# Kernel optimization log

Hardware: AMD Instinct MI355X
Metric: run time of the kernel (lower is better)

The kernel has to match this reference:

```python
import jax, jax.numpy as jnp
import numpy as np

N_NODES = 50000
N_EDGES = 640000
D = 128
L = 3


def setup_inputs() -> dict:
    key = jax.random.key(0)
    k1, k2, k3, k4 = jax.random.split(key, 4)
    x = jax.random.normal(k1, (N_NODES, D), dtype=jnp.float32)
    # Glorot-ish scale so activations stay O(1) across 3 layers
    Ws = jax.random.normal(k2, (L, D, D), dtype=jnp.float32) * (1.0 / np.sqrt(D))
    bs = jnp.zeros((L, D), dtype=jnp.float32)
    edge_src = jax.random.randint(k3, (N_EDGES,), 0, N_NODES, dtype=jnp.int32)
    edge_dst = jax.random.randint(k4, (N_EDGES,), 0, N_NODES, dtype=jnp.int32)
    return {"x": x, "Ws": Ws, "bs": bs, "edge_src": edge_src, "edge_dst": edge_dst}


def reference(x, Ws, bs, edge_src, edge_dst):
    n = x.shape[0]
    ones = jnp.ones(edge_src.shape[0], dtype=x.dtype)
    # degrees, clamped to 1 as in dgl GraphConv(norm='both')
    deg_out = jnp.maximum(jax.ops.segment_sum(ones, edge_src, num_segments=n), 1.0)
    deg_in = jnp.maximum(jax.ops.segment_sum(ones, edge_dst, num_segments=n), 1.0)
    inv_sqrt_out = jax.lax.rsqrt(deg_out)[:, None]  # [N,1]
    inv_sqrt_in = jax.lax.rsqrt(deg_in)[:, None]    # [N,1]
    for l in range(Ws.shape[0]):
        h = x * inv_sqrt_out                         # src normalization
        msg = h[edge_src]                            # [E,D] gather
        agg = jax.ops.segment_sum(msg, edge_dst, num_segments=n)  # [N,D] scatter-add
        h = agg * inv_sqrt_in                        # dst normalization
        x = jax.nn.relu(h @ Ws[l] + bs[l])           # linear + ReLU
    return x
```

## Files before the change

### kernel.cpp

```cpp
#include <hip/hip_runtime.h>
#include <hip/hip_fp16.h>

typedef __attribute__((ext_vector_type(8))) _Float16 half8;
typedef __attribute__((ext_vector_type(4))) float f32x4;
typedef unsigned int u32;
typedef unsigned short u16;
typedef unsigned long long u64;

#define ELL_PAD 64
#define BKT 128
#define BKT_SH 7
#define EPB 2048
#define NAMAX 512
#define RUNCAP 3072


__global__ __launch_bounds__(256) void initpack(int* __restrict__ deg_out,
                                                u32* __restrict__ xz0,
                                                u32* __restrict__ xz1,
                                                const float* __restrict__ Ws,
                                                _Float16* __restrict__ Whi,
                                                _Float16* __restrict__ Wlo,
                                                int N, int padU32, int zb, int packTotal) {
  int b = blockIdx.x;
  if (b < zb) {
    int i = b * 256 + threadIdx.x;
    if (i < N) deg_out[i] = 0;
    if (b == 0) {
      for (int j = threadIdx.x; j < padU32; j += 256) { xz0[j] = 0; xz1[j] = 0; }
    }
    return;
  }
  int i = (b - zb) * 256 + threadIdx.x;
  if (i < packTotal) {
    int lane  = i & 63;
    int kstep = (i >> 6) & 3;
    int ntile = (i >> 8) & 7;
    int layer = i >> 11;
    int nn = ntile * 16 + (lane & 15);
    int k0 = kstep * 32 + (lane >> 4) * 8;
    const float* W = Ws + (size_t)layer * 128 * 128;
    size_t base = (size_t)i * 8;
    for (int j = 0; j < 8; j++) {
      float v = W[(k0 + j) * 128 + nn];
      _Float16 hi = (_Float16)v;
      Whi[base + j] = hi;
      Wlo[base + j] = (_Float16)(v - (float)hi);
    }
  }
}


__global__ __launch_bounds__(512) void parta(const int* __restrict__ esrc,
                                             const int* __restrict__ edst,
                                             int* __restrict__ deg_out,
                                             u32* __restrict__ part,
                                             u32* __restrict__ runTab,
                                             int E, int NB) {
  __shared__ u32 hist[512];
  __shared__ u32 stage[EPB];
  __shared__ u32 scanA[512];
  int a = blockIdx.x;
  int e0 = a * EPB;
  int e1 = min(E, e0 + EPB);
  int len = e1 - e0;
  int tid = threadIdx.x;
  if (tid <= NB) hist[tid] = 0;
  __syncthreads();
  for (int i = e0 + tid; i < e1; i += 512) {
    int s = esrc[i];
    int d = edst[i];
    atomicAdd(&deg_out[s], 1);
    atomicAdd(&hist[d >> BKT_SH], 1u);
  }
  __syncthreads();
  u32 myc = (tid < NB) ? hist[tid] : 0;
  scanA[tid] = myc;
  __syncthreads();
  for (int off = 1; off < NB; off <<= 1) {
    u32 t = scanA[tid] + ((tid >= off) ? scanA[tid - off] : 0);
    __syncthreads();
    scanA[tid] = t;
    __syncthreads();
  }
  u32 excl = scanA[tid] - myc;
  u32* rt = runTab + (size_t)a * (NB + 1);
  if (tid < NB) { rt[tid] = excl; hist[tid] = excl; }
  if (tid == 0) rt[NB] = (u32)len;
  __syncthreads();
  for (int i = e0 + tid; i < e1; i += 512) {
    int s = esrc[i];
    int d = edst[i];
    u32 p = atomicAdd(&hist[d >> BKT_SH], 1u);
    stage[p] = (u32)s | ((u32)(d & (BKT - 1)) << 16);
  }
  __syncthreads();
  u32* op = part + (size_t)a * EPB;
  for (int j = tid; j < len; j += 512) op[j] = stage[j];
}


__global__ __launch_bounds__(512) void partb(const u32* __restrict__ part,
                                             const u32* __restrict__ runTab,
                                             int* __restrict__ deg_in,
                                             u16* __restrict__ ell,
                                             int N, int NA, int NB) {
  __shared__ u16 slice[BKT * ELL_PAD];
  __shared__ u32 cnt2[BKT * 17];
  __shared__ u32 roff[NAMAX + 1];
  __shared__ u32 rbase[NAMAX];
  __shared__ u16 runid[RUNCAP];
  __shared__ u32 pstage[RUNCAP];
  __shared__ u32 scanA[512];
  int b = blockIdx.x;
  int base = b * BKT;
  int hi = min(BKT, N - base);
  if (hi <= 0) return;
  int tid = threadIdx.x;

  u32 nv = ((u32)N << 16) | (u32)N;
  u32* s32 = (u32*)slice;
  for (int j = tid; j < BKT * (ELL_PAD / 2); j += 512) s32[j] = nv;
  for (int j = tid; j < BKT * 17; j += 512) cnt2[j] = 0;
  u32 mylen = 0;
  if (tid < NA) {
    u32 s = runTab[(size_t)tid * (NB + 1) + b];
    u32 e = runTab[(size_t)tid * (NB + 1) + b + 1];
    mylen = e - s;
    rbase[tid] = (u32)tid * EPB + s;
  }
  scanA[tid] = mylen;
  __syncthreads();
  for (int off = 1; off < NA + 1; off <<= 1) {
    u32 t = scanA[tid] + ((tid >= off) ? scanA[tid - off] : 0);
    __syncthreads();
    scanA[tid] = t;
    __syncthreads();
  }
  if (tid <= NA) roff[tid] = scanA[tid] - mylen;
  __syncthreads();
  int T = (int)roff[NA];
  for (int a = tid; a < NA; a += 512) {
    u32 s0 = roff[a];
    u32 l  = roff[a + 1] - s0;
    for (u32 k = 0; k < l; k++)
      if (s0 + k < RUNCAP) runid[s0 + k] = (u16)a;
  }
  __syncthreads();
  for (int i = tid; i < T; i += 512) {
    int a;
    if (i < RUNCAP) a = runid[i];
    else {
      int lo = 0, hh = NA;
      while (hh - lo > 1) { int mid = (lo + hh) >> 1; if (roff[mid] <= (u32)i) lo = mid; else hh = mid; }
      a = lo;
    }
    u32 pair = part[(size_t)rbase[a] + ((u32)i - roff[a])];
    if (i < RUNCAP) pstage[i] = pair;
    u32 dl  = pair >> 16;
    u32 src = pair & 0xFFFFu;
    atomicAdd(&cnt2[dl * 17 + (src >> 12)], 1u);
  }
  __syncthreads();
  if (tid < BKT) {
    u32 run = 0;
    for (int bk = 0; bk < 16; bk++) {
      u32 t = cnt2[tid * 17 + bk];
      cnt2[tid * 17 + bk] = run;
      run += t;
    }
    if (tid < hi) deg_in[base + tid] = (int)run;
  }
  __syncthreads();
  for (int i = tid; i < T; i += 512) {
    u32 pair;
    if (i < RUNCAP) pair = pstage[i];
    else {
      int lo = 0, hh = NA;
      while (hh - lo > 1) { int mid = (lo + hh) >> 1; if (roff[mid] <= (u32)i) lo = mid; else hh = mid; }
      pair = part[(size_t)rbase[lo] + ((u32)i - roff[lo])];
    }
    u32 dl  = pair >> 16;
    u32 src = pair & 0xFFFFu;
    u32 p = atomicAdd(&cnt2[dl * 17 + (src >> 12)], 1u);
    if (p < ELL_PAD) slice[dl * ELL_PAD + p] = (u16)src;
  }
  __syncthreads();
  u32* eg = (u32*)(ell + (size_t)base * ELL_PAD);
  for (int j = tid; j < hi * (ELL_PAD / 2); j += 512) eg[j] = s32[j];
}


__global__ __launch_bounds__(256) void xscale(const float* __restrict__ x,
                                              const int* __restrict__ deg_out,
                                              __half2* __restrict__ xh, int n64) {
  int gid = blockIdx.x * 256 + threadIdx.x;
  if (gid >= n64) return;
  int row = gid >> 6;
  int d = deg_out[row]; if (d < 1) d = 1;
  float s = rsqrtf((float)d);
  float2 v = ((const float2*)x)[gid];
  xh[gid] = __floats2half2_rn(v.x * s, v.y * s);
}


__global__ __launch_bounds__(512) void layer16(const _Float16* __restrict__ xh,
                                               const int* __restrict__ deg_in,
                                               const u16* __restrict__ ell,
                                               const _Float16* __restrict__ Whi,
                                               const _Float16* __restrict__ Wlo,
                                               const float* __restrict__ bias,
                                               const int* __restrict__ deg_out,
                                               __half* __restrict__ out16,
                                               float* __restrict__ out32, int n) {
  __shared__ _Float16 As[16 * 136];
  const int wave = threadIdx.x >> 6;
  const int lane = threadIdx.x & 63;
  const int sub  = lane & 15;
  const int grp  = lane >> 4;
  const int sh   = grp << 4;
  const u32 sub16 = (u32)sub * 16u;
  const int rowBase = blockIdx.x * 16;
  const char* __restrict__ xb = (const char*)xh;

  {
    int r0 = rowBase + wave * 2, r1 = r0 + 1;
    int d0 = (r0 < n) ? deg_in[r0] : 0;
    int d1 = (r1 < n) ? deg_in[r1] : 0;
    int l0 = d0 > ELL_PAD ? ELL_PAD : d0;
    int l1 = d1 > ELL_PAD ? ELL_PAD : d1;
    int t0 = (l0 + 3) & ~3;
    int t1 = (l1 + 3) & ~3;
    const u16* ep0 = ell + (u32)(r0 < n ? r0 : 0) * ELL_PAD;
    const u16* ep1 = ell + (u32)(r1 < n ? r1 : 0) * ELL_PAD;

    float a0[8] = {0.f, 0.f, 0.f, 0.f, 0.f, 0.f, 0.f, 0.f};
    float a1[8] = {0.f, 0.f, 0.f, 0.f, 0.f, 0.f, 0.f, 0.f};

    int m = t0 < t1 ? t0 : t1;
    int e = 0;
    for (; e + 8 <= m; e += 8) {
      u64 wa0 = *(const u64*)&ep0[e];
      u64 wa1 = *(const u64*)&ep0[e + 4];
      u64 wb0 = *(const u64*)&ep1[e];
      u64 wb1 = *(const u64*)&ep1[e + 4];
      u32 ia0 = ((u32)(wa0 >> sh) & 0xFFFFu) * 256u + sub16;
      u32 ia1 = ((u32)(wa1 >> sh) & 0xFFFFu) * 256u + sub16;
      u32 ib0 = ((u32)(wb0 >> sh) & 0xFFFFu) * 256u + sub16;
      u32 ib1 = ((u32)(wb1 >> sh) & 0xFFFFu) * 256u + sub16;
      half8 va0 = *(const half8*)(xb + ia0);
      half8 va1 = *(const half8*)(xb + ia1);
      half8 vb0 = *(const half8*)(xb + ib0);
      half8 vb1 = *(const half8*)(xb + ib1);
#pragma unroll
      for (int j = 0; j < 8; j++) {
        a0[j] += (float)va0[j] + (float)va1[j];
        a1[j] += (float)vb0[j] + (float)vb1[j];
      }
    }
    for (; e < m; e += 4) {
      u64 wa = *(const u64*)&ep0[e];
      u64 wb = *(const u64*)&ep1[e];
      u32 ia = ((u32)(wa >> sh) & 0xFFFFu) * 256u + sub16;
      u32 ib = ((u32)(wb >> sh) & 0xFFFFu) * 256u + sub16;
      half8 va = *(const half8*)(xb + ia);
      half8 vb = *(const half8*)(xb + ib);
#pragma unroll
      for (int j = 0; j < 8; j++) { a0[j] += (float)va[j]; a1[j] += (float)vb[j]; }
    }
    for (int ea = m; ea < t0; ea += 4) {
      u64 wa = *(const u64*)&ep0[ea];
      u32 ia = ((u32)(wa >> sh) & 0xFFFFu) * 256u + sub16;
      half8 va = *(const half8*)(xb + ia);
#pragma unroll
      for (int j = 0; j < 8; j++) a0[j] += (float)va[j];
    }
    for (int eb = m; eb < t1; eb += 4) {
      u64 wb = *(const u64*)&ep1[eb];
      u32 ib = ((u32)(wb >> sh) & 0xFFFFu) * 256u + sub16;
      half8 vb = *(const half8*)(xb + ib);
#pragma unroll
      for (int j = 0; j < 8; j++) a1[j] += (float)vb[j];
    }

#pragma unroll
    for (int j = 0; j < 8; j++) {
      a0[j] += __shfl_xor(a0[j], 16, 64);
      a0[j] += __shfl_xor(a0[j], 32, 64);
      a1[j] += __shfl_xor(a1[j], 16, 64);
      a1[j] += __shfl_xor(a1[j], 32, 64);
    }

    float si0 = rsqrtf((float)(d0 < 1 ? 1 : d0));
    float si1 = rsqrtf((float)(d1 < 1 ? 1 : d1));
    if (grp == 0) {
      half8 h0, h1;
#pragma unroll
      for (int j = 0; j < 8; j++) {
        h0[j] = (_Float16)(a0[j] * si0);
        h1[j] = (_Float16)(a1[j] * si1);
      }
      *(half8*)&As[(wave * 2 + 0) * 136 + sub * 8] = h0;
      *(half8*)&As[(wave * 2 + 1) * 136 + sub * 8] = h1;
    }
  }
  __syncthreads();

  f32x4 acc = (f32x4){0.f, 0.f, 0.f, 0.f};
#pragma unroll
  for (int ks = 0; ks < 4; ks++) {
    half8 a  = *(const half8*)&As[(size_t)sub * 136 + ks * 32 + grp * 8];
    half8 bh = *(const half8*)&Whi[((wave * 4 + ks) * 64 + lane) * 8];
    half8 bl = *(const half8*)&Wlo[((wave * 4 + ks) * 64 + lane) * 8];
    acc = __builtin_amdgcn_mfma_f32_16x16x32_f16(a, bh, acc, 0, 0, 0);
    acc = __builtin_amdgcn_mfma_f32_16x16x32_f16(a, bl, acc, 0, 0, 0);
  }

  const int r0c = rowBase + grp * 4;
  const int col = wave * 16 + sub;
  const float bv = bias[col];
#pragma unroll
  for (int r = 0; r < 4; r++) {
    int row = r0c + r;
    if (row < n) {
      float v = fmaxf(acc[r] + bv, 0.f);
      if (out16) {
        int d = deg_out[row]; if (d < 1) d = 1;
        out16[(size_t)row * 128 + col] = __float2half(v * rsqrtf((float)d));
      } else {
        out32[(size_t)row * 128 + col] = v;
      }
    }
  }
}


extern "C" void kernel_launch(void* const* d_in, const int* in_sizes, int n_in,
                              void* d_out, int out_size, void* d_ws, size_t ws_size,
                              hipStream_t stream) {
  const float* x   = (const float*)d_in[0];
  const float* Ws  = (const float*)d_in[1];
  const float* bs  = (const float*)d_in[2];
  const int* esrc  = (const int*)d_in[3];
  const int* edst  = (const int*)d_in[4];

  const int D = 128;
  const int N = in_sizes[0] / D;
  const int E = in_sizes[3];
  const int L = in_sizes[1] / (D * D);
  const int Npad = ((N + 15) / 16) * 16;
  const int NA = (E + EPB - 1) / EPB;
  const int NB = (N + BKT - 1) / BKT;

  char* base = (char*)d_ws;
  size_t off = 0;
  auto alloc = [&](size_t bytes) {
    char* p = base + off;
    off = (off + bytes + 255) & ~(size_t)255;
    return p;
  };
  int*      deg_out = (int*)alloc((size_t)N * 4);
  int*      deg_in  = (int*)alloc((size_t)N * 4);
  u16*      ell     = (u16*)alloc((size_t)N * ELL_PAD * 2);
  _Float16* Whi     = (_Float16*)alloc((size_t)L * 16384 * 2);
  _Float16* Wlo     = (_Float16*)alloc((size_t)L * 16384 * 2);
  _Float16* xh0     = (_Float16*)alloc((size_t)(Npad + 16) * 128 * 2);
  _Float16* xh1     = (_Float16*)alloc((size_t)(Npad + 16) * 128 * 2);
  u32*      part    = (u32*)alloc((size_t)NA * EPB * 4);
  u32*      runTab  = (u32*)alloc((size_t)NA * (NB + 1) * 4);

  const int zb = (N + 255) / 256;
  const int packTotal = L * 2048;
  const int packB = (packTotal + 255) / 256;
  const int padU32 = 16 * 64;

  initpack<<<dim3(zb + packB), dim3(256), 0, stream>>>(
      deg_out,
      (u32*)(xh0 + (size_t)N * 128), (u32*)(xh1 + (size_t)N * 128),
      Ws, Whi, Wlo, N, padU32, zb, packTotal);
  parta<<<dim3(NA), dim3(512), 0, stream>>>(
      esrc, edst, deg_out, part, runTab, E, NB);
  partb<<<dim3(NB), dim3(512), 0, stream>>>(
      part, runTab, deg_in, ell, N, NA, NB);
  xscale<<<dim3((N * 64 + 255) / 256), dim3(256), 0, stream>>>(
      x, deg_out, (__half2*)xh0, N * 64);

  float* outf = (float*)d_out;
  _Float16* ping[2] = {xh0, xh1};
  const dim3 lgrid(Npad / 16), lblk(512);

  for (int l = 0; l < L; l++) {
    bool last = (l == L - 1);
    layer16<<<lgrid, lblk, 0, stream>>>(
        (const _Float16*)ping[l & 1], deg_in, ell,
        Whi + (size_t)l * 16384, Wlo + (size_t)l * 16384,
        bs + (size_t)l * D, deg_out,
        last ? nullptr : (__half*)ping[(l + 1) & 1],
        last ? outf : nullptr, N);
  }
}
```

Measured before the change: 241.6 us.

## Sort rows by in-degree so each layer block processes similar-degree nodes

Builds a degree histogram in partb, prefix-sums it descending, and produces a permutation that groups nodes by clamped in-degree. Each layer block then gathers and transforms 16 rows of similar degree, so the two rows paired per wave have matched loop lengths and blocks get more uniform work, starting with the heaviest. The cost is two extra small kernels and an extra indirection per row. It also gives up locality, since consecutive output rows are now scattered and written non-contiguously.

```diff
diff --git a/kernel.cpp b/kernel.cpp
--- a/kernel.cpp
+++ b/kernel.cpp
@@ -16,6 +16,7 @@
 
 
 __global__ __launch_bounds__(256) void initpack(int* __restrict__ deg_out,
+                                                int* __restrict__ dbins,
                                                 u32* __restrict__ xz0,
                                                 u32* __restrict__ xz1,
                                                 const float* __restrict__ Ws,
@@ -27,6 +28,7 @@
     int i = b * 256 + threadIdx.x;
     if (i < N) deg_out[i] = 0;
     if (b == 0) {
+      if (threadIdx.x < 65) dbins[threadIdx.x] = 0;
       for (int j = threadIdx.x; j < padU32; j += 256) { xz0[j] = 0; xz1[j] = 0; }
     }
     return;
@@ -104,6 +106,7 @@
                                              const u32* __restrict__ runTab,
                                              int* __restrict__ deg_in,
                                              u16* __restrict__ ell,
+                                             int* __restrict__ dbins,
                                              int N, int NA, int NB) {
   __shared__ u16 slice[BKT * ELL_PAD];
   __shared__ u32 cnt2[BKT * 17];
@@ -112,6 +115,7 @@
   __shared__ u16 runid[RUNCAP];
   __shared__ u32 pstage[RUNCAP];
   __shared__ u32 scanA[512];
+  __shared__ int dh[65];
   int b = blockIdx.x;
   int base = b * BKT;
   int hi = min(BKT, N - base);
@@ -122,6 +126,7 @@
   u32* s32 = (u32*)slice;
   for (int j = tid; j < BKT * (ELL_PAD / 2); j += 512) s32[j] = nv;
   for (int j = tid; j < BKT * 17; j += 512) cnt2[j] = 0;
+  if (tid < 65) dh[tid] = 0;
   u32 mylen = 0;
   if (tid < NA) {
     u32 s = runTab[(size_t)tid * (NB + 1) + b];
@@ -169,7 +174,11 @@
       cnt2[tid * 17 + bk] = run;
       run += t;
     }
-    if (tid < hi) deg_in[base + tid] = (int)run;
+    if (tid < hi) {
+      deg_in[base + tid] = (int)run;
+      int dc = run > 64u ? 64 : (int)run;
+      atomicAdd(&dh[dc], 1);
+    }
   }
   __syncthreads();
   for (int i = tid; i < T; i += 512) {
@@ -188,6 +197,36 @@
   __syncthreads();
   u32* eg = (u32*)(ell + (size_t)base * ELL_PAD);
   for (int j = tid; j < hi * (ELL_PAD / 2); j += 512) eg[j] = s32[j];
+  for (int j = tid; j < 65; j += 512) atomicAdd(&dbins[j], dh[j]);
+}
+
+
+__global__ __launch_bounds__(128) void dprefix(int* __restrict__ dbins) {
+  __shared__ int v[65];
+  int t = threadIdx.x;
+  if (t < 65) v[t] = dbins[t];
+  __syncthreads();
+  if (t == 0) {
+    int run = 0;
+    for (int d = 64; d >= 0; d--) { int c = v[d]; v[d] = run; run += c; }
+  }
+  __syncthreads();
+  if (t < 65) dbins[t] = v[t];
+}
+
+
+__global__ __launch_bounds__(256) void dplace(const int* __restrict__ deg_in,
+                                              int* __restrict__ dbins,
+                                              int* __restrict__ perm,
+                                              int N, int Npad) {
+  int i = blockIdx.x * 256 + threadIdx.x;
+  if (i < N) {
+    int d = deg_in[i]; if (d > 64) d = 64;
+    int pos = atomicAdd(&dbins[d], 1);
+    perm[pos] = i;
+  } else if (i < Npad) {
+    perm[i] = N;
+  }
 }
 
 
@@ -207,6 +246,7 @@
 __global__ __launch_bounds__(512) void layer16(const _Float16* __restrict__ xh,
                                                const int* __restrict__ deg_in,
                                                const u16* __restrict__ ell,
+                                               const int* __restrict__ perm,
                                                const _Float16* __restrict__ Whi,
                                                const _Float16* __restrict__ Wlo,
                                                const float* __restrict__ bias,
@@ -214,6 +254,7 @@
                                                __half* __restrict__ out16,
                                                float* __restrict__ out32, int n) {
   __shared__ _Float16 As[16 * 136];
+  __shared__ int rmap[16];
   const int wave = threadIdx.x >> 6;
   const int lane = threadIdx.x & 63;
   const int sub  = lane & 15;
@@ -223,8 +264,11 @@
   const int rowBase = blockIdx.x * 16;
   const char* __restrict__ xb = (const char*)xh;
 
+  if (threadIdx.x < 16) rmap[threadIdx.x] = perm[rowBase + threadIdx.x];
+
   {
-    int r0 = rowBase + wave * 2, r1 = r0 + 1;
+    int r0 = perm[rowBase + wave * 2];
+    int r1 = perm[rowBase + wave * 2 + 1];
     int d0 = (r0 < n) ? deg_in[r0] : 0;
     int d1 = (r1 < n) ? deg_in[r1] : 0;
     int l0 = d0 > ELL_PAD ? ELL_PAD : d0;
@@ -316,12 +360,11 @@
     acc = __builtin_amdgcn_mfma_f32_16x16x32_f16(a, bl, acc, 0, 0, 0);
   }
 
-  const int r0c = rowBase + grp * 4;
   const int col = wave * 16 + sub;
   const float bv = bias[col];
 #pragma unroll
   for (int r = 0; r < 4; r++) {
-    int row = r0c + r;
+    int row = rmap[grp * 4 + r];
     if (row < n) {
       float v = fmaxf(acc[r] + bv, 0.f);
       if (out16) {
@@ -361,6 +404,8 @@
   };
   int*      deg_out = (int*)alloc((size_t)N * 4);
   int*      deg_in  = (int*)alloc((size_t)N * 4);
+  int*      perm    = (int*)alloc((size_t)Npad * 4);
+  int*      dbins   = (int*)alloc(80 * 4);
   u16*      ell     = (u16*)alloc((size_t)N * ELL_PAD * 2);
   _Float16* Whi     = (_Float16*)alloc((size_t)L * 16384 * 2);
   _Float16* Wlo     = (_Float16*)alloc((size_t)L * 16384 * 2);
@@ -375,13 +420,16 @@
   const int padU32 = 16 * 64;
 
   initpack<<<dim3(zb + packB), dim3(256), 0, stream>>>(
-      deg_out,
+      deg_out, dbins,
       (u32*)(xh0 + (size_t)N * 128), (u32*)(xh1 + (size_t)N * 128),
       Ws, Whi, Wlo, N, padU32, zb, packTotal);
   parta<<<dim3(NA), dim3(512), 0, stream>>>(
       esrc, edst, deg_out, part, runTab, E, NB);
   partb<<<dim3(NB), dim3(512), 0, stream>>>(
-      part, runTab, deg_in, ell, N, NA, NB);
+      part, runTab, deg_in, ell, dbins, N, NA, NB);
+  dprefix<<<dim3(1), dim3(128), 0, stream>>>(dbins);
+  dplace<<<dim3((Npad + 255) / 256), dim3(256), 0, stream>>>(
+      deg_in, dbins, perm, N, Npad);
   xscale<<<dim3((N * 64 + 255) / 256), dim3(256), 0, stream>>>(
       x, deg_out, (__half2*)xh0, N * 64);
 
@@ -392,7 +440,7 @@
   for (int l = 0; l < L; l++) {
     bool last = (l == L - 1);
     layer16<<<lgrid, lblk, 0, stream>>>(
-        (const _Float16*)ping[l & 1], deg_in, ell,
+        (const _Float16*)ping[l & 1], deg_in, ell, perm,
         Whi + (size_t)l * 16384, Wlo + (size_t)l * 16384,
         bs + (size_t)l * D, deg_out,
         last ? nullptr : (__half*)ping[(l + 1) & 1],
```

Result: slower. 400.5 us (+65.7%).

## Fuse x scaling into partb, prefetch first ELL gathers, hoist weight loads

Applied to the files above, without the earlier changes.

The separate xscale kernel is folded into the tail of partb, which saves one launch. In layer16, the first 24 ELL slots per row are loaded unconditionally up front, so all their gathers are in flight at once. The remainder loops start at slot 24, and padding entries point at a zeroed sentinel row, so the extra loads are harmless. Weight fragments for the MFMA are loaded before the barrier so they overlap with the aggregation. The cost is higher register pressure and wasted gathers for low-degree rows.

```diff
diff --git a/kernel.cpp b/kernel.cpp
--- a/kernel.cpp
+++ b/kernel.cpp
@@ -13,6 +13,7 @@
 #define EPB 2048
 #define NAMAX 512
 #define RUNCAP 3072
+#define PRE 24
 
 
 __global__ __launch_bounds__(256) void initpack(int* __restrict__ deg_out,
@@ -102,8 +103,11 @@
 
 __global__ __launch_bounds__(512) void partb(const u32* __restrict__ part,
                                              const u32* __restrict__ runTab,
+                                             const float* __restrict__ x,
+                                             const int* __restrict__ deg_out,
                                              int* __restrict__ deg_in,
                                              u16* __restrict__ ell,
+                                             __half2* __restrict__ xh,
                                              int N, int NA, int NB) {
   __shared__ u16 slice[BKT * ELL_PAD];
   __shared__ u32 cnt2[BKT * 17];
@@ -188,19 +192,18 @@
   __syncthreads();
   u32* eg = (u32*)(ell + (size_t)base * ELL_PAD);
   for (int j = tid; j < hi * (ELL_PAD / 2); j += 512) eg[j] = s32[j];
-}
-
-
-__global__ __launch_bounds__(256) void xscale(const float* __restrict__ x,
-                                              const int* __restrict__ deg_out,
-                                              __half2* __restrict__ xh, int n64) {
-  int gid = blockIdx.x * 256 + threadIdx.x;
-  if (gid >= n64) return;
-  int row = gid >> 6;
-  int d = deg_out[row]; if (d < 1) d = 1;
-  float s = rsqrtf((float)d);
-  float2 v = ((const float2*)x)[gid];
-  xh[gid] = __floats2half2_rn(v.x * s, v.y * s);
+  float* sc = (float*)scanA;
+  if (tid < hi) {
+    int d = deg_out[base + tid]; if (d < 1) d = 1;
+    sc[tid] = rsqrtf((float)d);
+  }
+  __syncthreads();
+  for (int j = tid; j < hi * 64; j += 512) {
+    int r = j >> 6, c = j & 63;
+    float s = sc[r];
+    float2 v = ((const float2*)x)[(size_t)(base + r) * 64 + c];
+    xh[(size_t)(base + r) * 64 + c] = __floats2half2_rn(v.x * s, v.y * s);
+  }
 }
 
 
@@ -229,58 +232,53 @@
     int d1 = (r1 < n) ? deg_in[r1] : 0;
     int l0 = d0 > ELL_PAD ? ELL_PAD : d0;
     int l1 = d1 > ELL_PAD ? ELL_PAD : d1;
+    const u16* ep0 = ell + (u32)(r0 < n ? r0 : 0) * ELL_PAD;
+    const u16* ep1 = ell + (u32)(r1 < n ? r1 : 0) * ELL_PAD;
+
+    u64 w0[PRE / 4], w1[PRE / 4];
+#pragma unroll
+    for (int k = 0; k < PRE / 4; k++) {
+      w0[k] = *(const u64*)&ep0[k * 4];
+      w1[k] = *(const u64*)&ep1[k * 4];
+    }
+    u32 ia[PRE / 4], ib[PRE / 4];
+#pragma unroll
+    for (int k = 0; k < PRE / 4; k++) {
+      ia[k] = ((u32)(w0[k] >> sh) & 0xFFFFu) * 256u + sub16;
+      ib[k] = ((u32)(w1[k] >> sh) & 0xFFFFu) * 256u + sub16;
+    }
+    half8 ga[PRE / 4], gb[PRE / 4];
+#pragma unroll
+    for (int k = 0; k < PRE / 4; k++) {
+      ga[k] = *(const half8*)(xb + ia[k]);
+      gb[k] = *(const half8*)(xb + ib[k]);
+    }
+
+    float a0[8] = {0.f, 0.f, 0.f, 0.f, 0.f, 0.f, 0.f, 0.f};
+    float a1[8] = {0.f, 0.f, 0.f, 0.f, 0.f, 0.f, 0.f, 0.f};
+#pragma unroll
+    for (int k = 0; k < PRE / 4; k++)
+#pragma unroll
+      for (int j = 0; j < 8; j++) {
+        a0[j] += (float)ga[k][j];
+        a1[j] += (float)gb[k][j];
+      }
+
     int t0 = (l0 + 3) & ~3;
     int t1 = (l1 + 3) & ~3;
-    const u16* ep0 = ell + (u32)(r0 < n ? r0 : 0) * ELL_PAD;
-    const u16* ep1 = ell + (u32)(r1 < n ? r1 : 0) * ELL_PAD;
-
-    float a0[8] = {0.f, 0.f, 0.f, 0.f, 0.f, 0.f, 0.f, 0.f};
-    float a1[8] = {0.f, 0.f, 0.f, 0.f, 0.f, 0.f, 0.f, 0.f};
-
-    int m = t0 < t1 ? t0 : t1;
-    int e = 0;
-    for (; e + 8 <= m; e += 8) {
-      u64 wa0 = *(const u64*)&ep0[e];
-      u64 wa1 = *(const u64*)&ep0[e + 4];
-      u64 wb0 = *(const u64*)&ep1[e];
-      u64 wb1 = *(const u64*)&ep1[e + 4];
-      u32 ia0 = ((u32)(wa0 >> sh) & 0xFFFFu) * 256u + sub16;
-      u32 ia1 = ((u32)(wa1 >> sh) & 0xFFFFu) * 256u + sub16;
-      u32 ib0 = ((u32)(wb0 >> sh) & 0xFFFFu) * 256u + sub16;
-      u32 ib1 = ((u32)(wb1 >> sh) & 0xFFFFu) * 256u + sub16;
-      half8 va0 = *(const half8*)(xb + ia0);
-      half8 va1 = *(const half8*)(xb + ia1);
-      half8 vb0 = *(const half8*)(xb + ib0);
-      half8 vb1 = *(const half8*)(xb + ib1);
-#pragma unroll
-      for (int j = 0; j < 8; j++) {
-        a0[j] += (float)va0[j] + (float)va1[j];
-        a1[j] += (float)vb0[j] + (float)vb1[j];
-      }
-    }
-    for (; e < m; e += 4) {
-      u64 wa = *(const u64*)&ep0[e];
-      u64 wb = *(const u64*)&ep1[e];
-      u32 ia = ((u32)(wa >> sh) & 0xFFFFu) * 256u + sub16;
-      u32 ib = ((u32)(wb >> sh) & 0xFFFFu) * 256u + sub16;
-      half8 va = *(const half8*)(xb + ia);
-      half8 vb = *(const half8*)(xb + ib);
-#pragma unroll
-      for (int j = 0; j < 8; j++) { a0[j] += (float)va[j]; a1[j] += (float)vb[j]; }
-    }
-    for (int ea = m; ea < t0; ea += 4) {
-      u64 wa = *(const u64*)&ep0[ea];
-      u32 ia = ((u32)(wa >> sh) & 0xFFFFu) * 256u + sub16;
-      half8 va = *(const half8*)(xb + ia);
-#pragma unroll
-      for (int j = 0; j < 8; j++) a0[j] += (float)va[j];
-    }
-    for (int eb = m; eb < t1; eb += 4) {
-      u64 wb = *(const u64*)&ep1[eb];
-      u32 ib = ((u32)(wb >> sh) & 0xFFFFu) * 256u + sub16;
-      half8 vb = *(const half8*)(xb + ib);
-#pragma unroll
-      for (int j = 0; j < 8; j++) a1[j] += (float)vb[j];
+    for (int e = PRE; e < t0; e += 4) {
+      u64 w = *(const u64*)&ep0[e];
+      u32 i0 = ((u32)(w >> sh) & 0xFFFFu) * 256u + sub16;
+      half8 v = *(const half8*)(xb + i0);
+#pragma unroll
+      for (int j = 0; j < 8; j++) a0[j] += (float)v[j];
+    }
+    for (int e = PRE; e < t1; e += 4) {
+      u64 w = *(const u64*)&ep1[e];
+      u32 i0 = ((u32)(w >> sh) & 0xFFFFu) * 256u + sub16;
+      half8 v = *(const half8*)(xb + i0);
+#pragma unroll
+      for (int j = 0; j < 8; j++) a1[j] += (float)v[j];
     }
 
 #pragma unroll
@@ -304,16 +302,21 @@
       *(half8*)&As[(wave * 2 + 1) * 136 + sub * 8] = h1;
     }
   }
+
+  half8 wh[4], wl[4];
+#pragma unroll
+  for (int ks = 0; ks < 4; ks++) {
+    wh[ks] = *(const half8*)&Whi[((wave * 4 + ks) * 64 + lane) * 8];
+    wl[ks] = *(const half8*)&Wlo[((wave * 4 + ks) * 64 + lane) * 8];
+  }
   __syncthreads();
 
   f32x4 acc = (f32x4){0.f, 0.f, 0.f, 0.f};
 #pragma unroll
   for (int ks = 0; ks < 4; ks++) {
-    half8 a  = *(const half8*)&As[(size_t)sub * 136 + ks * 32 + grp * 8];
-    half8 bh = *(const half8*)&Whi[((wave * 4 + ks) * 64 + lane) * 8];
-    half8 bl = *(const half8*)&Wlo[((wave * 4 + ks) * 64 + lane) * 8];
-    acc = __builtin_amdgcn_mfma_f32_16x16x32_f16(a, bh, acc, 0, 0, 0);
-    acc = __builtin_amdgcn_mfma_f32_16x16x32_f16(a, bl, acc, 0, 0, 0);
+    half8 a = *(const half8*)&As[(size_t)sub * 136 + ks * 32 + grp * 8];
+    acc = __builtin_amdgcn_mfma_f32_16x16x32_f16(a, wh[ks], acc, 0, 0, 0);
+    acc = __builtin_amdgcn_mfma_f32_16x16x32_f16(a, wl[ks], acc, 0, 0, 0);
   }
 
   const int r0c = rowBase + grp * 4;
@@ -381,9 +384,7 @@
   parta<<<dim3(NA), dim3(512), 0, stream>>>(
       esrc, edst, deg_out, part, runTab, E, NB);
   partb<<<dim3(NB), dim3(512), 0, stream>>>(
-      part, runTab, deg_in, ell, N, NA, NB);
-  xscale<<<dim3((N * 64 + 255) / 256), dim3(256), 0, stream>>>(
-      x, deg_out, (__half2*)xh0, N * 64);
+      part, runTab, x, deg_out, deg_in, ell, (__half2*)xh0, N, NA, NB);
 
   float* outf = (float*)d_out;
   _Float16* ping[2] = {xh0, xh1};
```

Result: no change. 241.7 us (+0.0%).

## Split fused gather+GEMM layer into separate gather and 64-row MFMA kernels

Applied to the files above, without the earlier changes.

The fused per-16-row layer kernel is split into a gather kernel (8 rows per 256-thread block) that writes the normalized aggregate in fp16 to a global buffer, and a GEMM kernel that processes 64 rows per block with the W fragments held in registers. The aim is better occupancy for the latency-bound gather and less repeated W loading per row tile. The cost is an extra global round trip for the aggregate and one more launch per layer. Separately, the xscale kernel is folded into partb so that launch is removed.

```diff
diff --git a/kernel.cpp b/kernel.cpp
--- a/kernel.cpp
+++ b/kernel.cpp
@@ -102,8 +102,11 @@
 
 __global__ __launch_bounds__(512) void partb(const u32* __restrict__ part,
                                              const u32* __restrict__ runTab,
+                                             const float* __restrict__ x,
+                                             const int* __restrict__ deg_out,
                                              int* __restrict__ deg_in,
                                              u16* __restrict__ ell,
+                                             __half2* __restrict__ xh,
                                              int N, int NA, int NB) {
   __shared__ u16 slice[BKT * ELL_PAD];
   __shared__ u32 cnt2[BKT * 17];
@@ -188,147 +191,165 @@
   __syncthreads();
   u32* eg = (u32*)(ell + (size_t)base * ELL_PAD);
   for (int j = tid; j < hi * (ELL_PAD / 2); j += 512) eg[j] = s32[j];
-}
-
-
-__global__ __launch_bounds__(256) void xscale(const float* __restrict__ x,
-                                              const int* __restrict__ deg_out,
-                                              __half2* __restrict__ xh, int n64) {
-  int gid = blockIdx.x * 256 + threadIdx.x;
-  if (gid >= n64) return;
-  int row = gid >> 6;
-  int d = deg_out[row]; if (d < 1) d = 1;
-  float s = rsqrtf((float)d);
-  float2 v = ((const float2*)x)[gid];
-  xh[gid] = __floats2half2_rn(v.x * s, v.y * s);
-}
-
-
-__global__ __launch_bounds__(512) void layer16(const _Float16* __restrict__ xh,
-                                               const int* __restrict__ deg_in,
-                                               const u16* __restrict__ ell,
-                                               const _Float16* __restrict__ Whi,
-                                               const _Float16* __restrict__ Wlo,
-                                               const float* __restrict__ bias,
-                                               const int* __restrict__ deg_out,
-                                               __half* __restrict__ out16,
-                                               float* __restrict__ out32, int n) {
-  __shared__ _Float16 As[16 * 136];
-  const int wave = threadIdx.x >> 6;
-  const int lane = threadIdx.x & 63;
+  float* sc = (float*)scanA;
+  if (tid < hi) {
+    int d = deg_out[base + tid]; if (d < 1) d = 1;
+    sc[tid] = rsqrtf((float)d);
+  }
+  __syncthreads();
+  for (int j = tid; j < hi * 64; j += 512) {
+    int r = j >> 6, c = j & 63;
+    float s = sc[r];
+    float2 v = ((const float2*)x)[(size_t)(base + r) * 64 + c];
+    xh[(size_t)(base + r) * 64 + c] = __floats2half2_rn(v.x * s, v.y * s);
+  }
+}
+
+
+__global__ __launch_bounds__(256) void gath8(const _Float16* __restrict__ xh,
+                                             const int* __restrict__ deg_in,
+                                             const u16* __restrict__ ell,
+                                             _Float16* __restrict__ agg, int n) {
+  const int wave = (int)threadIdx.x >> 6;
+  const int lane = (int)threadIdx.x & 63;
   const int sub  = lane & 15;
   const int grp  = lane >> 4;
   const int sh   = grp << 4;
   const u32 sub16 = (u32)sub * 16u;
-  const int rowBase = blockIdx.x * 16;
   const char* __restrict__ xb = (const char*)xh;
 
-  {
-    int r0 = rowBase + wave * 2, r1 = r0 + 1;
-    int d0 = (r0 < n) ? deg_in[r0] : 0;
-    int d1 = (r1 < n) ? deg_in[r1] : 0;
-    int l0 = d0 > ELL_PAD ? ELL_PAD : d0;
-    int l1 = d1 > ELL_PAD ? ELL_PAD : d1;
-    int t0 = (l0 + 3) & ~3;
-    int t1 = (l1 + 3) & ~3;
-    const u16* ep0 = ell + (u32)(r0 < n ? r0 : 0) * ELL_PAD;
-    const u16* ep1 = ell + (u32)(r1 < n ? r1 : 0) * ELL_PAD;
-
-    float a0[8] = {0.f, 0.f, 0.f, 0.f, 0.f, 0.f, 0.f, 0.f};
-    float a1[8] = {0.f, 0.f, 0.f, 0.f, 0.f, 0.f, 0.f, 0.f};
-
-    int m = t0 < t1 ? t0 : t1;
-    int e = 0;
-    for (; e + 8 <= m; e += 8) {
-      u64 wa0 = *(const u64*)&ep0[e];
-      u64 wa1 = *(const u64*)&ep0[e + 4];
-      u64 wb0 = *(const u64*)&ep1[e];
-      u64 wb1 = *(const u64*)&ep1[e + 4];
-      u32 ia0 = ((u32)(wa0 >> sh) & 0xFFFFu) * 256u + sub16;
-      u32 ia1 = ((u32)(wa1 >> sh) & 0xFFFFu) * 256u + sub16;
-      u32 ib0 = ((u32)(wb0 >> sh) & 0xFFFFu) * 256u + sub16;
-      u32 ib1 = ((u32)(wb1 >> sh) & 0xFFFFu) * 256u + sub16;
-      half8 va0 = *(const half8*)(xb + ia0);
-      half8 va1 = *(const half8*)(xb + ia1);
-      half8 vb0 = *(const half8*)(xb + ib0);
-      half8 vb1 = *(const half8*)(xb + ib1);
-#pragma unroll
-      for (int j = 0; j < 8; j++) {
-        a0[j] += (float)va0[j] + (float)va1[j];
-        a1[j] += (float)vb0[j] + (float)vb1[j];
-      }
-    }
-    for (; e < m; e += 4) {
-      u64 wa = *(const u64*)&ep0[e];
-      u64 wb = *(const u64*)&ep1[e];
-      u32 ia = ((u32)(wa >> sh) & 0xFFFFu) * 256u + sub16;
-      u32 ib = ((u32)(wb >> sh) & 0xFFFFu) * 256u + sub16;
-      half8 va = *(const half8*)(xb + ia);
-      half8 vb = *(const half8*)(xb + ib);
-#pragma unroll
-      for (int j = 0; j < 8; j++) { a0[j] += (float)va[j]; a1[j] += (float)vb[j]; }
-    }
-    for (int ea = m; ea < t0; ea += 4) {
-      u64 wa = *(const u64*)&ep0[ea];
-      u32 ia = ((u32)(wa >> sh) & 0xFFFFu) * 256u + sub16;
-      half8 va = *(const half8*)(xb + ia);
-#pragma unroll
-      for (int j = 0; j < 8; j++) a0[j] += (float)va[j];
-    }
-    for (int eb = m; eb < t1; eb += 4) {
-      u64 wb = *(const u64*)&ep1[eb];
-      u32 ib = ((u32)(wb >> sh) & 0xFFFFu) * 256u + sub16;
-      half8 vb = *(const half8*)(xb + ib);
-#pragma unroll
-      for (int j = 0; j < 8; j++) a1[j] += (float)vb[j];
-    }
-
+  int r0 = blockIdx.x * 8 + wave * 2, r1 = r0 + 1;
+  int d0 = (r0 < n) ? deg_in[r0] : 0;
+  int d1 = (r1 < n) ? deg_in[r1] : 0;
+  int l0 = d0 > ELL_PAD ? ELL_PAD : d0;
+  int l1 = d1 > ELL_PAD ? ELL_PAD : d1;
+  int t0 = (l0 + 3) & ~3;
+  int t1 = (l1 + 3) & ~3;
+  const u16* ep0 = ell + (u32)(r0 < n ? r0 : 0) * ELL_PAD;
+  const u16* ep1 = ell + (u32)(r1 < n ? r1 : 0) * ELL_PAD;
+
+  float a0[8] = {0.f, 0.f, 0.f, 0.f, 0.f, 0.f, 0.f, 0.f};
+  float a1[8] = {0.f, 0.f, 0.f, 0.f, 0.f, 0.f, 0.f, 0.f};
+
+  int m = t0 < t1 ? t0 : t1;
+  int e = 0;
+  for (; e + 8 <= m; e += 8) {
+    u64 wa0 = *(const u64*)&ep0[e];
+    u64 wa1 = *(const u64*)&ep0[e + 4];
+    u64 wb0 = *(const u64*)&ep1[e];
+    u64 wb1 = *(const u64*)&ep1[e + 4];
+    u32 ia0 = ((u32)(wa0 >> sh) & 0xFFFFu) * 256u + sub16;
+    u32 ia1 = ((u32)(wa1 >> sh) & 0xFFFFu) * 256u + sub16;
+    u32 ib0 = ((u32)(wb0 >> sh) & 0xFFFFu) * 256u + sub16;
+    u32 ib1 = ((u32)(wb1 >> sh) & 0xFFFFu) * 256u + sub16;
+    half8 va0 = *(const half8*)(xb + ia0);
+    half8 va1 = *(const half8*)(xb + ia1);
+    half8 vb0 = *(const half8*)(xb + ib0);
+    half8 vb1 = *(const half8*)(xb + ib1);
 #pragma unroll
     for (int j = 0; j < 8; j++) {
-      a0[j] += __shfl_xor(a0[j], 16, 64);
-      a0[j] += __shfl_xor(a0[j], 32, 64);
-      a1[j] += __shfl_xor(a1[j], 16, 64);
-      a1[j] += __shfl_xor(a1[j], 32, 64);
-    }
-
-    float si0 = rsqrtf((float)(d0 < 1 ? 1 : d0));
-    float si1 = rsqrtf((float)(d1 < 1 ? 1 : d1));
-    if (grp == 0) {
-      half8 h0, h1;
-#pragma unroll
-      for (int j = 0; j < 8; j++) {
-        h0[j] = (_Float16)(a0[j] * si0);
-        h1[j] = (_Float16)(a1[j] * si1);
-      }
-      *(half8*)&As[(wave * 2 + 0) * 136 + sub * 8] = h0;
-      *(half8*)&As[(wave * 2 + 1) * 136 + sub * 8] = h1;
-    }
-  }
-  __syncthreads();
-
-  f32x4 acc = (f32x4){0.f, 0.f, 0.f, 0.f};
+      a0[j] += (float)va0[j] + (float)va1[j];
+      a1[j] += (float)vb0[j] + (float)vb1[j];
+    }
+  }
+  for (; e < m; e += 4) {
+    u64 wa = *(const u64*)&ep0[e];
+    u64 wb = *(const u64*)&ep1[e];
+    u32 ia = ((u32)(wa >> sh) & 0xFFFFu) * 256u + sub16;
+    u32 ib = ((u32)(wb >> sh) & 0xFFFFu) * 256u + sub16;
+    half8 va = *(const half8*)(xb + ia);
+    half8 vb = *(const half8*)(xb + ib);
+#pragma unroll
+    for (int j = 0; j < 8; j++) { a0[j] += (float)va[j]; a1[j] += (float)vb[j]; }
+  }
+  for (int ea = m; ea < t0; ea += 4) {
+    u64 wa = *(const u64*)&ep0[ea];
+    u32 ia = ((u32)(wa >> sh) & 0xFFFFu) * 256u + sub16;
+    half8 va = *(const half8*)(xb + ia);
+#pragma unroll
+    for (int j = 0; j < 8; j++) a0[j] += (float)va[j];
+  }
+  for (int eb = m; eb < t1; eb += 4) {
+    u64 wb = *(const u64*)&ep1[eb];
+    u32 ib = ((u32)(wb >> sh) & 0xFFFFu) * 256u + sub16;
+    half8 vb = *(const half8*)(xb + ib);
+#pragma unroll
+    for (int j = 0; j < 8; j++) a1[j] += (float)vb[j];
+  }
+
+#pragma unroll
+  for (int j = 0; j < 8; j++) {
+    a0[j] += __shfl_xor(a0[j], 16, 64);
+    a0[j] += __shfl_xor(a0[j], 32, 64);
+    a1[j] += __shfl_xor(a1[j], 16, 64);
+    a1[j] += __shfl_xor(a1[j], 32, 64);
+  }
+
+  float si0 = rsqrtf((float)(d0 < 1 ? 1 : d0));
+  float si1 = rsqrtf((float)(d1 < 1 ? 1 : d1));
+  if (grp == 0) {
+    half8 h0, h1;
+#pragma unroll
+    for (int j = 0; j < 8; j++) {
+      h0[j] = (_Float16)(a0[j] * si0);
+      h1[j] = (_Float16)(a1[j] * si1);
+    }
+    *(half8*)&agg[(size_t)r0 * 128 + sub * 8] = h0;
+    *(half8*)&agg[(size_t)r1 * 128 + sub * 8] = h1;
+  }
+}
+
+
+__global__ __launch_bounds__(512) void mm64(const _Float16* __restrict__ agg,
+                                            const _Float16* __restrict__ Whi,
+                                            const _Float16* __restrict__ Wlo,
+                                            const float* __restrict__ bias,
+                                            const int* __restrict__ deg_out,
+                                            __half* __restrict__ out16,
+                                            float* __restrict__ out32, int n) {
+  __shared__ _Float16 As[64 * 136];
+  const int wave = (int)threadIdx.x >> 6;
+  const int lane = (int)threadIdx.x & 63;
+  const int sub  = lane & 15;
+  const int grp  = lane >> 4;
+  const int rowBase = blockIdx.x * 64;
+
+  for (int j = threadIdx.x; j < 64 * 16; j += 512) {
+    int r = j >> 4, c = j & 15;
+    *(half8*)&As[r * 136 + c * 8] =
+        *(const half8*)&agg[(size_t)(rowBase + r) * 128 + c * 8];
+  }
+  half8 wh[4], wl[4];
 #pragma unroll
   for (int ks = 0; ks < 4; ks++) {
-    half8 a  = *(const half8*)&As[(size_t)sub * 136 + ks * 32 + grp * 8];
-    half8 bh = *(const half8*)&Whi[((wave * 4 + ks) * 64 + lane) * 8];
-    half8 bl = *(const half8*)&Wlo[((wave * 4 + ks) * 64 + lane) * 8];
-    acc = __builtin_amdgcn_mfma_f32_16x16x32_f16(a, bh, acc, 0, 0, 0);
-    acc = __builtin_amdgcn_mfma_f32_16x16x32_f16(a, bl, acc, 0, 0, 0);
-  }
-
-  const int r0c = rowBase + grp * 4;
+    wh[ks] = *(const half8*)&Whi[((wave * 4 + ks) * 64 + lane) * 8];
+    wl[ks] = *(const half8*)&Wlo[((wave * 4 + ks) * 64 + lane) * 8];
+  }
+  __syncthreads();
+
   const int col = wave * 16 + sub;
   const float bv = bias[col];
 #pragma unroll
-  for (int r = 0; r < 4; r++) {
-    int row = r0c + r;
-    if (row < n) {
-      float v = fmaxf(acc[r] + bv, 0.f);
-      if (out16) {
-        int d = deg_out[row]; if (d < 1) d = 1;
-        out16[(size_t)row * 128 + col] = __float2half(v * rsqrtf((float)d));
-      } else {
-        out32[(size_t)row * 128 + col] = v;
+  for (int rt = 0; rt < 4; rt++) {
+    f32x4 acc = (f32x4){0.f, 0.f, 0.f, 0.f};
+#pragma unroll
+    for (int ks = 0; ks < 4; ks++) {
+      half8 a = *(const half8*)&As[(rt * 16 + sub) * 136 + ks * 32 + grp * 8];
+      acc = __builtin_amdgcn_mfma_f32_16x16x32_f16(a, wh[ks], acc, 0, 0, 0);
+      acc = __builtin_amdgcn_mfma_f32_16x16x32_f16(a, wl[ks], acc, 0, 0, 0);
+    }
+    int r0c = rowBase + rt * 16 + grp * 4;
+#pragma unroll
+    for (int r = 0; r < 4; r++) {
+      int row = r0c + r;
+      if (row < n) {
+        float v = fmaxf(acc[r] + bv, 0.f);
+        if (out16) {
+          int d = deg_out[row]; if (d < 1) d = 1;
+          out16[(size_t)row * 128 + col] = __float2half(v * rsqrtf((float)d));
+        } else {
+          out32[(size_t)row * 128 + col] = v;
+        }
       }
     }
   }
@@ -348,7 +369,7 @@
   const int N = in_sizes[0] / D;
   const int E = in_sizes[3];
   const int L = in_sizes[1] / (D * D);
-  const int Npad = ((N + 15) / 16) * 16;
+  const int Npad = ((N + 63) / 64) * 64;
   const int NA = (E + EPB - 1) / EPB;
   const int NB = (N + BKT - 1) / BKT;
 
@@ -366,6 +387,7 @@
   _Float16* Wlo     = (_Float16*)alloc((size_t)L * 16384 * 2);
   _Float16* xh0     = (_Float16*)alloc((size_t)(Npad + 16) * 128 * 2);
   _Float16* xh1     = (_Float16*)alloc((size_t)(Npad + 16) * 128 * 2);
+  _Float16* agg     = (_Float16*)alloc((size_t)Npad * 128 * 2);
   u32*      part    = (u32*)alloc((size_t)NA * EPB * 4);
   u32*      runTab  = (u32*)alloc((size_t)NA * (NB + 1) * 4);
 
@@ -381,19 +403,17 @@
   parta<<<dim3(NA), dim3(512), 0, stream>>>(
       esrc, edst, deg_out, part, runTab, E, NB);
   partb<<<dim3(NB), dim3(512), 0, stream>>>(
-      part, runTab, deg_in, ell, N, NA, NB);
-  xscale<<<dim3((N * 64 + 255) / 256), dim3(256), 0, stream>>>(
-      x, deg_out, (__half2*)xh0, N * 64);
+      part, runTab, x, deg_out, deg_in, ell, (__half2*)xh0, N, NA, NB);
 
   float* outf = (float*)d_out;
   _Float16* ping[2] = {xh0, xh1};
-  const dim3 lgrid(Npad / 16), lblk(512);
 
   for (int l = 0; l < L; l++) {
     bool last = (l == L - 1);
-    layer16<<<lgrid, lblk, 0, stream>>>(
-        (const _Float16*)ping[l & 1], deg_in, ell,
-        Whi + (size_t)l * 16384, Wlo + (size_t)l * 16384,
+    gath8<<<dim3(Npad / 8), dim3(256), 0, stream>>>(
+        (const _Float16*)ping[l & 1], deg_in, ell, agg, N);
+    mm64<<<dim3(Npad / 64), dim3(512), 0, stream>>>(
+        agg, Whi + (size_t)l * 16384, Wlo + (size_t)l * 16384,
         bs + (size_t)l * D, deg_out,
         last ? nullptr : (__half*)ping[(l + 1) & 1],
         last ? outf : nullptr, N);
```

Result: no change. 243.8 us (+0.9%).
